# Kernel tuning notes

Measured on AMD Instinct MI355X. Metric: run time of the kernel, lower is better.

The kernel has to match this reference:

```python
import jax, jax.numpy as jnp
import numpy as np

N_EMBD = 1024
N_HEAD = 16
HEAD_SIZE = N_EMBD // N_HEAD
SEQ_LEN = 2048


def setup_inputs() -> dict:
    key = jax.random.key(0)
    k_x, k_wa, k_ba, k_wp, k_bp = jax.random.split(key, 5)
    s = 0.02
    return {
        "x": jax.random.normal(k_x, (4, SEQ_LEN, N_EMBD), dtype=jnp.float32),
        "w_attn": jax.random.normal(k_wa, (N_EMBD, 3 * N_EMBD), dtype=jnp.float32) * s,
        "b_attn": jax.random.normal(k_ba, (3 * N_EMBD,), dtype=jnp.float32) * s,
        "w_proj": jax.random.normal(k_wp, (N_EMBD, N_EMBD), dtype=jnp.float32) * s,
        "b_proj": jax.random.normal(k_bp, (N_EMBD,), dtype=jnp.float32) * s,
    }


def reference(x, w_attn, b_attn, w_proj, b_proj):
    B, T, C = x.shape
    H, D = N_HEAD, HEAD_SIZE
    qkv = x @ w_attn + b_attn                      # [B,T,3C]
    q, k, v = jnp.split(qkv, 3, axis=-1)
    q = q.reshape(B, T, H, D).transpose(0, 2, 1, 3)  # [B,H,T,D]
    k = k.reshape(B, T, H, D).transpose(0, 2, 1, 3)
    v = v.reshape(B, T, H, D).transpose(0, 2, 1, 3)
    att = jnp.einsum('bhqd,bhkd->bhqk', q, k) / jnp.sqrt(jnp.float32(D))
    causal = jnp.tril(jnp.ones((T, T), dtype=bool))
    att = jnp.where(causal[None, None], att, jnp.float32(-jnp.inf))
    att = jax.nn.softmax(att, axis=-1)
    out = jnp.einsum('bhqk,bhkd->bhqd', att, v)    # [B,H,T,D]
    out = out.transpose(0, 2, 1, 3).reshape(B, T, C)
    return out @ w_proj + b_proj
```

## Files before the change

### kernel.cpp

```cpp
#include <hip/hip_runtime.h>

typedef short short8 __attribute__((ext_vector_type(8)));
typedef short short4v __attribute__((ext_vector_type(4)));
typedef float f32x4 __attribute__((ext_vector_type(4)));
typedef unsigned uint2v __attribute__((ext_vector_type(2)));

__device__ __forceinline__ float bf2f(short b) {
  unsigned u = ((unsigned)(unsigned short)b) << 16;
  return __builtin_bit_cast(float, u);
}
__device__ __forceinline__ short f2bf(float f) {
  unsigned u = __builtin_bit_cast(unsigned, f);
  u += 0x7fffu + ((u >> 16) & 1u);
  return (short)(u >> 16);
}
__device__ __forceinline__ unsigned cvt_pk_bf16(float lo, float hi) {
  unsigned r;
  asm("v_cvt_pk_bf16_f32 %0, %1, %2" : "=v"(r) : "v"(lo), "v"(hi));
  return r;
}

__device__ __forceinline__ void gload_lds16(const void* g, void* l) {
  __builtin_amdgcn_global_load_lds(
      (const __attribute__((address_space(1))) unsigned int*)g,
      (__attribute__((address_space(3))) unsigned int*)l, 16, 0, 0);
}

__device__ __forceinline__ short8 lds_frag(const short* tile, int row, int kc, int l4) {
  int chunk = (kc * 4 + l4) ^ (row & 7);
  return *(const short8*)&tile[row * 64 + chunk * 8];
}

__global__ __launch_bounds__(256) void k_convert_bf16(const float* __restrict__ in,
                                                      short* __restrict__ out, int n8) {
  int i = blockIdx.x * 256 + threadIdx.x;
  if (i >= n8) return;
  const float4* p = (const float4*)in;
  float4 a = p[2 * i], b = p[2 * i + 1];
  short8 o;
  o[0] = f2bf(a.x); o[1] = f2bf(a.y); o[2] = f2bf(a.z); o[3] = f2bf(a.w);
  o[4] = f2bf(b.x); o[5] = f2bf(b.y); o[6] = f2bf(b.z); o[7] = f2bf(b.w);
  ((short8*)out)[i] = o;
}

__global__ __launch_bounds__(256) void k_transpose_w(const float* __restrict__ w,
                                                     short* __restrict__ wT, int K, int N) {
  __shared__ float t[32][33];
  int nt = N >> 5;
  int rt = blockIdx.x / nt, ct = blockIdx.x % nt;
  int tx = threadIdx.x & 31, ty = threadIdx.x >> 5;
#pragma unroll
  for (int i = 0; i < 4; ++i) {
    int r = ty * 4 + i;
    t[r][tx] = w[(size_t)(rt * 32 + r) * N + ct * 32 + tx];
  }
  __syncthreads();
#pragma unroll
  for (int i = 0; i < 4; ++i) {
    int r = ty * 4 + i;
    wT[(size_t)(ct * 32 + r) * K + rt * 32 + tx] = f2bf(t[tx][r]);
  }
}

template <bool BF16OUT>
__global__ __launch_bounds__(512, 1) void k_gemm8p(const short* __restrict__ A,
                                                   const short* __restrict__ Bt,
                                                   const float* __restrict__ bias,
                                                   void* __restrict__ Cout,
                                                   int M, int N, int K) {
  __shared__ __align__(16) short Ab[2][256 * 64];
  __shared__ __align__(16) short Bb[2][256 * 64];
  int nt = N >> 8;
  int nwg = gridDim.x;
  int bid = blockIdx.x;
  int swz = (bid & 7) * (nwg >> 3) + (bid >> 3);
  int mt = swz / nt, ct = swz % nt;
  int tid = threadIdx.x, w = tid >> 6, lane = tid & 63;
  int l15 = lane & 15, l4 = lane >> 4;
  int wm = w >> 2, wn = w & 3;
  const short* Abase = A + (size_t)mt * 256 * K;
  const short* Bbase = Bt + (size_t)ct * 256 * K;
  int NT = K >> 6;

  int srow = lane >> 3;
  int slc = (lane & 7) ^ srow;

  auto stage = [&](const short* gbase, short* dstTile, int kt, int half) {
#pragma unroll
    for (int i = 0; i < 2; ++i) {
      int rowg = half * 128 + i * 64 + w * 8;
      gload_lds16(gbase + (size_t)(rowg + srow) * K + kt * 64 + slc * 8,
                  dstTile + (size_t)rowg * 64);
    }
  };

  f32x4 acc[8][4];
#pragma unroll
  for (int m = 0; m < 8; ++m)
#pragma unroll
    for (int n = 0; n < 4; ++n) acc[m][n] = f32x4{0.f, 0.f, 0.f, 0.f};

  stage(Bbase, &Bb[0][0], 0, 0);
  stage(Bbase, &Bb[0][0], 0, 1);
  stage(Abase, &Ab[0][0], 0, 0);
  stage(Abase, &Ab[0][0], 0, 1);
  stage(Bbase, &Bb[1][0], 1, 0);
  stage(Bbase, &Bb[1][0], 1, 1);
  stage(Abase, &Ab[1][0], 1, 0);
  stage(Abase, &Ab[1][0], 1, 1);
  asm volatile("s_waitcnt vmcnt(8)" ::: "memory");
  __builtin_amdgcn_s_barrier();

  for (int t = 0; t < NT; ++t) {
    int b = t & 1;
    const short* At = &Ab[b][0];
    const short* Btl = &Bb[b][0];
    short* Aw = &Ab[b][0];
    short* Bw = &Bb[b][0];
    bool pre = (t + 2 < NT);

    short8 aflo[4][2], bflo[2][2], bfhi[2][2], afhi[4][2];
#pragma unroll
    for (int mq = 0; mq < 4; ++mq)
#pragma unroll
      for (int kc = 0; kc < 2; ++kc)
        aflo[mq][kc] = lds_frag(At, wm * 128 + mq * 16 + l15, kc, l4);
#pragma unroll
    for (int nq = 0; nq < 2; ++nq)
#pragma unroll
      for (int kc = 0; kc < 2; ++kc)
        bflo[nq][kc] = lds_frag(Btl, wn * 64 + nq * 16 + l15, kc, l4);
    __builtin_amdgcn_s_barrier();
    asm volatile("s_waitcnt lgkmcnt(0)" ::: "memory");
    __builtin_amdgcn_sched_barrier(0);
    __builtin_amdgcn_s_setprio(1);
#pragma unroll
    for (int mq = 0; mq < 4; ++mq)
#pragma unroll
      for (int nq = 0; nq < 2; ++nq)
#pragma unroll
        for (int kc = 0; kc < 2; ++kc)
          acc[mq][nq] = __builtin_amdgcn_mfma_f32_16x16x32_bf16(aflo[mq][kc], bflo[nq][kc], acc[mq][nq], 0, 0, 0);
    __builtin_amdgcn_s_setprio(0);
    __builtin_amdgcn_s_barrier();

#pragma unroll
    for (int nq = 0; nq < 2; ++nq)
#pragma unroll
      for (int kc = 0; kc < 2; ++kc)
        bfhi[nq][kc] = lds_frag(Btl, wn * 64 + 32 + nq * 16 + l15, kc, l4);
    __builtin_amdgcn_s_barrier();
    asm volatile("s_waitcnt lgkmcnt(0)" ::: "memory");
    __builtin_amdgcn_sched_barrier(0);
    __builtin_amdgcn_s_setprio(1);
#pragma unroll
    for (int mq = 0; mq < 4; ++mq)
#pragma unroll
      for (int nq = 0; nq < 2; ++nq)
#pragma unroll
        for (int kc = 0; kc < 2; ++kc)
          acc[mq][2 + nq] = __builtin_amdgcn_mfma_f32_16x16x32_bf16(aflo[mq][kc], bfhi[nq][kc], acc[mq][2 + nq], 0, 0, 0);
    __builtin_amdgcn_s_setprio(0);
    __builtin_amdgcn_s_barrier();

#pragma unroll
    for (int mq = 0; mq < 4; ++mq)
#pragma unroll
      for (int kc = 0; kc < 2; ++kc)
        afhi[mq][kc] = lds_frag(At, wm * 128 + 64 + mq * 16 + l15, kc, l4);
    if (pre) {
      stage(Bbase, Bw, t + 2, 0);
      stage(Bbase, Bw, t + 2, 1);
    }
    __builtin_amdgcn_s_barrier();
    asm volatile("s_waitcnt lgkmcnt(0)" ::: "memory");
    __builtin_amdgcn_sched_barrier(0);
    __builtin_amdgcn_s_setprio(1);
#pragma unroll
    for (int mq = 0; mq < 4; ++mq)
#pragma unroll
      for (int nq = 0; nq < 2; ++nq)
#pragma unroll
        for (int kc = 0; kc < 2; ++kc)
          acc[4 + mq][2 + nq] = __builtin_amdgcn_mfma_f32_16x16x32_bf16(afhi[mq][kc], bfhi[nq][kc], acc[4 + mq][2 + nq], 0, 0, 0);
    __builtin_amdgcn_s_setprio(0);
    __builtin_amdgcn_s_barrier();

    if (pre) {
      stage(Abase, Aw, t + 2, 0);
      stage(Abase, Aw, t + 2, 1);
    }
    __builtin_amdgcn_s_setprio(1);
#pragma unroll
    for (int mq = 0; mq < 4; ++mq)
#pragma unroll
      for (int nq = 0; nq < 2; ++nq)
#pragma unroll
        for (int kc = 0; kc < 2; ++kc)
          acc[4 + mq][nq] = __builtin_amdgcn_mfma_f32_16x16x32_bf16(afhi[mq][kc], bflo[nq][kc], acc[4 + mq][nq], 0, 0, 0);
    __builtin_amdgcn_s_setprio(0);
    if (pre) {
      asm volatile("s_waitcnt vmcnt(8)" ::: "memory");
    } else if (t + 1 < NT) {
      asm volatile("s_waitcnt vmcnt(0)" ::: "memory");
    }
    __builtin_amdgcn_s_barrier();
  }

#pragma unroll
  for (int m = 0; m < 8; ++m) {
#pragma unroll
    for (int n = 0; n < 4; ++n) {
      int row = mt * 256 + wm * 128 + m * 16 + l4 * 4;
      int col = ct * 256 + wn * 64 + n * 16 + l15;
      float bv = bias[col];
#pragma unroll
      for (int j = 0; j < 4; ++j) {
        float v = acc[m][n][j] + bv;
        if constexpr (BF16OUT)
          ((short*)Cout)[(size_t)(row + j) * N + col] = f2bf(v);
        else
          ((float*)Cout)[(size_t)(row + j) * N + col] = v;
      }
    }
  }
}

template <bool BF16OUT>
__global__ __launch_bounds__(256) void k_gemm_bt(const short* __restrict__ A,
                                                 const short* __restrict__ Bt,
                                                 const float* __restrict__ bias,
                                                 void* __restrict__ Cout,
                                                 int M, int N, int K) {
  __shared__ __align__(16) short As[128 * 32];
  __shared__ __align__(16) short Bs[128 * 32];
  int nt = N >> 7;
  int mt = blockIdx.x / nt, ct = blockIdx.x % nt;
  int tid = threadIdx.x, w = tid >> 6, lane = tid & 63;
  int l15 = lane & 15, l4 = lane >> 4;
  int wr = (w >> 1) * 64, wc = (w & 1) * 64;
  const short* Abase = A + (size_t)mt * 128 * K;
  const short* Bbase = Bt + (size_t)ct * 128 * K;
  f32x4 acc[4][4];
#pragma unroll
  for (int m = 0; m < 4; ++m)
#pragma unroll
    for (int n = 0; n < 4; ++n) acc[m][n] = f32x4{0.f, 0.f, 0.f, 0.f};

  for (int kt = 0; kt < K; kt += 32) {
    __syncthreads();
#pragma unroll
    for (int i = 0; i < 2; ++i) {
      int idx = (w * 2 + i) * 64 + lane;
      gload_lds16(Abase + (size_t)(idx >> 2) * K + kt + (idx & 3) * 8, &As[(w * 2 + i) * 512]);
      gload_lds16(Bbase + (size_t)(idx >> 2) * K + kt + (idx & 3) * 8, &Bs[(w * 2 + i) * 512]);
    }
    __syncthreads();
    short8 af[4], bfr[4];
#pragma unroll
    for (int m = 0; m < 4; ++m) af[m] = *(const short8*)&As[(wr + m * 16 + l15) * 32 + l4 * 8];
#pragma unroll
    for (int n = 0; n < 4; ++n) bfr[n] = *(const short8*)&Bs[(wc + n * 16 + l15) * 32 + l4 * 8];
#pragma unroll
    for (int m = 0; m < 4; ++m)
#pragma unroll
      for (int n = 0; n < 4; ++n)
        acc[m][n] = __builtin_amdgcn_mfma_f32_16x16x32_bf16(af[m], bfr[n], acc[m][n], 0, 0, 0);
  }

#pragma unroll
  for (int m = 0; m < 4; ++m) {
#pragma unroll
    for (int n = 0; n < 4; ++n) {
      int row = mt * 128 + wr + m * 16 + l4 * 4;
      int col = ct * 128 + wc + n * 16 + l15;
      float bv = bias[col];
#pragma unroll
      for (int j = 0; j < 4; ++j) {
        float v = acc[m][n][j] + bv;
        if constexpr (BF16OUT)
          ((short*)Cout)[(size_t)(row + j) * N + col] = f2bf(v);
        else
          ((float*)Cout)[(size_t)(row + j) * N + col] = v;
      }
    }
  }
}

__global__ __launch_bounds__(256) void k_transpose_v(const short* __restrict__ qkv,
                                                     short* __restrict__ vT) {
  __shared__ __align__(16) short t[64][72];
  int blk = blockIdx.x;
  int tt = blk & 31, bh = blk >> 5;
  int batch = bh >> 4, h = bh & 15;
  int tid = threadIdx.x;
  const short* base = qkv + (size_t)(batch * 2048 + tt * 64) * 3072 + 2048 + h * 64;
#pragma unroll
  for (int rep = 0; rep < 2; ++rep) {
    int idx = rep * 256 + tid;
    int r = idx >> 3, dc = idx & 7;
    *(short8*)&t[r][dc * 8] = *(const short8*)(base + (size_t)r * 3072 + dc * 8);
  }
  __syncthreads();
  short* obase = vT + (size_t)bh * 64 * 2048 + tt * 64;
#pragma unroll
  for (int rep = 0; rep < 2; ++rep) {
    int idx = rep * 256 + tid;
    int d = idx >> 3, tc = idx & 7;
    short8 o;
#pragma unroll
    for (int i = 0; i < 8; ++i) o[i] = t[tc * 8 + i][d];
    *(short8*)(obase + (size_t)d * 2048 + tc * 8) = o;
  }
}

__global__ __launch_bounds__(256, 2) void k_attn(const short* __restrict__ qkv,
                                                 const short* __restrict__ vT,
                                                 short* __restrict__ out) {
  constexpr int T = 2048, C3 = 3072;
  __shared__ __align__(16) short Kl[2][64 * 72];
  __shared__ __align__(16) short P_lds[4][32 * 72];
  int bp = blockIdx.x & 7, bh = blockIdx.x >> 3;
  int batch = bh >> 4, h = bh & 15;
  int tid = threadIdx.x, w = tid >> 6, lane = tid & 63;
  int l15 = lane & 15, l4 = lane >> 4;

  int qt[2];
  qt[0] = 63 - (bp * 4 + w);
  qt[1] = bp * 4 + w;
  int lim[2] = {qt[0] >> 1, qt[1] >> 1};
  int ktb = (63 - bp * 4) >> 1;

  const short* kbase = qkv + (size_t)(batch * T) * C3 + 1024 + h * 64;
  const short* vbase = vT + (size_t)bh * 64 * T;

  int sr0 = tid >> 3, sr1 = 32 + (tid >> 3), sdc = (tid & 7) * 8;

  const float SCL = 0.18033688f;
  short8 qf[2][2][2];
#pragma unroll
  for (int t = 0; t < 2; ++t)
#pragma unroll
    for (int qc = 0; qc < 2; ++qc) {
      const short* qrow = qkv + (size_t)(batch * T + qt[t] * 32 + qc * 16 + l15) * C3 + h * 64;
#pragma unroll
      for (int kc = 0; kc < 2; ++kc) {
        short8 v = *(const short8*)(qrow + kc * 32 + l4 * 8);
#pragma unroll
        for (int i = 0; i < 8; ++i) v[i] = f2bf(bf2f(v[i]) * SCL);
        qf[t][qc][kc] = v;
      }
    }

  f32x4 o_[2][2][4];
  float l_[2][2];
#pragma unroll
  for (int t = 0; t < 2; ++t)
#pragma unroll
    for (int qc = 0; qc < 2; ++qc) {
      l_[t][qc] = 0.f;
#pragma unroll
      for (int dt = 0; dt < 4; ++dt) o_[t][qc][dt] = f32x4{0.f, 0.f, 0.f, 0.f};
    }

  {
    short8 a = *(const short8*)(kbase + (size_t)sr0 * C3 + sdc);
    short8 b = *(const short8*)(kbase + (size_t)sr1 * C3 + sdc);
    *(short8*)&Kl[0][sr0 * 72 + sdc] = a;
    *(short8*)&Kl[0][sr1 * 72 + sdc] = b;
  }
  __syncthreads();

  int cur = 0;
  for (int kt = 0; kt <= ktb; ++kt) {
    bool more = (kt < ktb);
    bool act0 = (kt <= lim[0]), act1 = (kt <= lim[1]);

    short8 pre0, pre1;
    if (more) {
      pre0 = *(const short8*)(kbase + (size_t)((kt + 1) * 64 + sr0) * C3 + sdc);
      pre1 = *(const short8*)(kbase + (size_t)((kt + 1) * 64 + sr1) * C3 + sdc);
    }

    const short* Kb = &Kl[cur][0];
    short8 kf[4][2];
#pragma unroll
    for (int kvt = 0; kvt < 4; ++kvt)
#pragma unroll
      for (int kc = 0; kc < 2; ++kc)
        kf[kvt][kc] = *(const short8*)(Kb + (kvt * 16 + l15) * 72 + kc * 32 + l4 * 8);

    short8 vf[4][2];
#pragma unroll
    for (int dt = 0; dt < 4; ++dt)
#pragma unroll
      for (int kc = 0; kc < 2; ++kc)
        vf[dt][kc] = *(const short8*)(vbase + (size_t)(dt * 16 + l15) * T + kt * 64 + kc * 32 + l4 * 8);

#pragma unroll
    for (int t = 0; t < 2; ++t) {
      bool act = (t == 0) ? act0 : act1;
      if (!act) continue;
      short* pb = &P_lds[w][0];

#pragma unroll
      for (int qc = 0; qc < 2; ++qc) {
        f32x4 s[4];
#pragma unroll
        for (int kvt = 0; kvt < 4; ++kvt) s[kvt] = f32x4{0.f, 0.f, 0.f, 0.f};
        __builtin_amdgcn_s_setprio(1);
#pragma unroll
        for (int kvt = 0; kvt < 4; ++kvt)
#pragma unroll
          for (int kc = 0; kc < 2; ++kc)
            s[kvt] = __builtin_amdgcn_mfma_f32_16x16x32_bf16(kf[kvt][kc], qf[t][qc][kc], s[kvt], 0, 0, 0);
        __builtin_amdgcn_s_setprio(0);

        if (kt == lim[t]) {
          int qg = qt[t] * 32 + qc * 16 + l15;
#pragma unroll
          for (int kvt = 0; kvt < 4; ++kvt)
#pragma unroll
            for (int j = 0; j < 4; ++j) {
              int kg = kt * 64 + kvt * 16 + l4 * 4 + j;
              if (kg > qg) s[kvt][j] = -1e30f;
            }
        }

        float ls = 0.f;
#pragma unroll
        for (int kvt = 0; kvt < 4; ++kvt) {
          float p0 = exp2f(s[kvt][0]);
          float p1 = exp2f(s[kvt][1]);
          float p2 = exp2f(s[kvt][2]);
          float p3 = exp2f(s[kvt][3]);
          ls += (p0 + p1) + (p2 + p3);
          unsigned lo = cvt_pk_bf16(p0, p1);
          unsigned hi = cvt_pk_bf16(p2, p3);
          *(uint2v*)(pb + (qc * 16 + l15) * 72 + kvt * 16 + l4 * 4) = uint2v{lo, hi};
        }
        l_[t][qc] += ls;
      }

      asm volatile("s_waitcnt lgkmcnt(0)" ::: "memory");

      __builtin_amdgcn_s_setprio(1);
#pragma unroll
      for (int qc = 0; qc < 2; ++qc)
#pragma unroll
        for (int dt = 0; dt < 4; ++dt)
#pragma unroll
          for (int kc = 0; kc < 2; ++kc) {
            short8 pf = *(const short8*)(pb + (qc * 16 + l15) * 72 + kc * 32 + l4 * 8);
            o_[t][qc][dt] = __builtin_amdgcn_mfma_f32_16x16x32_bf16(vf[dt][kc], pf, o_[t][qc][dt], 0, 0, 0);
          }
      __builtin_amdgcn_s_setprio(0);
    }

    if (more) {
      *(short8*)&Kl[cur ^ 1][sr0 * 72 + sdc] = pre0;
      *(short8*)&Kl[cur ^ 1][sr1 * 72 + sdc] = pre1;
    }
    __syncthreads();
    cur ^= 1;
  }

#pragma unroll
  for (int t = 0; t < 2; ++t) {
#pragma unroll
    for (int qc = 0; qc < 2; ++qc) {
      float lt = l_[t][qc];
      lt += __shfl_xor(lt, 16);
      lt += __shfl_xor(lt, 32);
      float inv = 1.f / lt;
      size_t rowb = (size_t)(batch * T + qt[t] * 32 + qc * 16 + l15) * 1024 + h * 64;
#pragma unroll
      for (int dt = 0; dt < 4; ++dt) {
        short4v pk4;
#pragma unroll
        for (int j = 0; j < 4; ++j) pk4[j] = f2bf(o_[t][qc][dt][j] * inv);
        *(short4v*)(out + rowb + dt * 16 + l4 * 4) = pk4;
      }
    }
  }
}

extern "C" void kernel_launch(void* const* d_in, const int* in_sizes, int n_in,
                              void* d_out, int out_size, void* d_ws, size_t ws_size,
                              hipStream_t stream) {
  const float* x      = (const float*)d_in[0];
  const float* w_attn = (const float*)d_in[1];
  const float* b_attn = (const float*)d_in[2];
  const float* w_proj = (const float*)d_in[3];
  const float* b_proj = (const float*)d_in[4];
  float* out = (float*)d_out;

  char* ws = (char*)d_ws;
  short* xb   = (short*)(ws);
  short* waT  = (short*)(ws + 16777216);
  short* wpT  = (short*)(ws + 23068672);
  short* qkv  = (short*)(ws + 25165824);
  short* vT   = (short*)(ws + 75497472);
  short* attn = xb;

  k_convert_bf16<<<4096, 256, 0, stream>>>(x, xb, 1048576);
  k_transpose_w<<<32 * 96, 256, 0, stream>>>(w_attn, waT, 1024, 3072);
  k_transpose_w<<<32 * 32, 256, 0, stream>>>(w_proj, wpT, 1024, 1024);
  k_gemm8p<true><<<384, 512, 0, stream>>>(xb, waT, b_attn, qkv, 8192, 3072, 1024);
  k_transpose_v<<<2048, 256, 0, stream>>>(qkv, vT);
  k_attn<<<512, 256, 0, stream>>>(qkv, vT, attn);
  k_gemm_bt<false><<<64 * 8, 256, 0, stream>>>(attn, wpT, b_proj, out, 8192, 1024, 1024);
}
```

Before: 199.1 us.

## Halve attention query tile per wave and double block count for occupancy

Each wave in the attention kernel now processes 16-row query tiles instead of 32. The grid doubles to 1024 blocks, and launch bounds now allow 4 blocks per CU. Fewer accumulator registers and more resident waves are meant to improve latency hiding and load balance across CUs. The cost is more K/V tile loads from memory per query row, since each loaded tile feeds half as many queries.

```diff
diff --git a/kernel.cpp b/kernel.cpp
--- a/kernel.cpp
+++ b/kernel.cpp
@@ -314,22 +314,23 @@
   }
 }
 
-__global__ __launch_bounds__(256, 2) void k_attn(const short* __restrict__ qkv,
+__global__ __launch_bounds__(256, 4) void k_attn(const short* __restrict__ qkv,
                                                  const short* __restrict__ vT,
                                                  short* __restrict__ out) {
   constexpr int T = 2048, C3 = 3072;
   __shared__ __align__(16) short Kl[2][64 * 72];
-  __shared__ __align__(16) short P_lds[4][32 * 72];
-  int bp = blockIdx.x & 7, bh = blockIdx.x >> 3;
+  __shared__ __align__(16) short P_lds[4][16 * 72];
+  int bp = blockIdx.x & 15, bh = blockIdx.x >> 4;
   int batch = bh >> 4, h = bh & 15;
   int tid = threadIdx.x, w = tid >> 6, lane = tid & 63;
   int l15 = lane & 15, l4 = lane >> 4;
 
+  int x = bp * 4 + w;
   int qt[2];
-  qt[0] = 63 - (bp * 4 + w);
-  qt[1] = bp * 4 + w;
-  int lim[2] = {qt[0] >> 1, qt[1] >> 1};
-  int ktb = (63 - bp * 4) >> 1;
+  qt[0] = 127 - x;
+  qt[1] = x;
+  int lim[2] = {(qt[0] * 16 + 15) >> 6, (qt[1] * 16 + 15) >> 6};
+  int ktb = 31 - bp;
 
   const short* kbase = qkv + (size_t)(batch * T) * C3 + 1024 + h * 64;
   const short* vbase = vT + (size_t)bh * 64 * T;
@@ -337,31 +338,25 @@
   int sr0 = tid >> 3, sr1 = 32 + (tid >> 3), sdc = (tid & 7) * 8;
 
   const float SCL = 0.18033688f;
-  short8 qf[2][2][2];
+  short8 qf[2][2];
+#pragma unroll
+  for (int t = 0; t < 2; ++t) {
+    const short* qrow = qkv + (size_t)(batch * T + qt[t] * 16 + l15) * C3 + h * 64;
+#pragma unroll
+    for (int kc = 0; kc < 2; ++kc) {
+      short8 v = *(const short8*)(qrow + kc * 32 + l4 * 8);
+#pragma unroll
+      for (int i = 0; i < 8; ++i) v[i] = f2bf(bf2f(v[i]) * SCL);
+      qf[t][kc] = v;
+    }
+  }
+
+  f32x4 o_[2][4];
+  float l_[2] = {0.f, 0.f};
 #pragma unroll
   for (int t = 0; t < 2; ++t)
 #pragma unroll
-    for (int qc = 0; qc < 2; ++qc) {
-      const short* qrow = qkv + (size_t)(batch * T + qt[t] * 32 + qc * 16 + l15) * C3 + h * 64;
-#pragma unroll
-      for (int kc = 0; kc < 2; ++kc) {
-        short8 v = *(const short8*)(qrow + kc * 32 + l4 * 8);
-#pragma unroll
-        for (int i = 0; i < 8; ++i) v[i] = f2bf(bf2f(v[i]) * SCL);
-        qf[t][qc][kc] = v;
-      }
-    }
-
-  f32x4 o_[2][2][4];
-  float l_[2][2];
-#pragma unroll
-  for (int t = 0; t < 2; ++t)
-#pragma unroll
-    for (int qc = 0; qc < 2; ++qc) {
-      l_[t][qc] = 0.f;
-#pragma unroll
-      for (int dt = 0; dt < 4; ++dt) o_[t][qc][dt] = f32x4{0.f, 0.f, 0.f, 0.f};
-    }
+    for (int dt = 0; dt < 4; ++dt) o_[t][dt] = f32x4{0.f, 0.f, 0.f, 0.f};
 
   {
     short8 a = *(const short8*)(kbase + (size_t)sr0 * C3 + sdc);
@@ -397,63 +392,58 @@
       for (int kc = 0; kc < 2; ++kc)
         vf[dt][kc] = *(const short8*)(vbase + (size_t)(dt * 16 + l15) * T + kt * 64 + kc * 32 + l4 * 8);
 
+    short* pb = &P_lds[w][0];
 #pragma unroll
     for (int t = 0; t < 2; ++t) {
       bool act = (t == 0) ? act0 : act1;
       if (!act) continue;
-      short* pb = &P_lds[w][0];
-
-#pragma unroll
-      for (int qc = 0; qc < 2; ++qc) {
-        f32x4 s[4];
-#pragma unroll
-        for (int kvt = 0; kvt < 4; ++kvt) s[kvt] = f32x4{0.f, 0.f, 0.f, 0.f};
-        __builtin_amdgcn_s_setprio(1);
+
+      f32x4 s[4];
+#pragma unroll
+      for (int kvt = 0; kvt < 4; ++kvt) s[kvt] = f32x4{0.f, 0.f, 0.f, 0.f};
+      __builtin_amdgcn_s_setprio(1);
+#pragma unroll
+      for (int kvt = 0; kvt < 4; ++kvt)
+#pragma unroll
+        for (int kc = 0; kc < 2; ++kc)
+          s[kvt] = __builtin_amdgcn_mfma_f32_16x16x32_bf16(kf[kvt][kc], qf[t][kc], s[kvt], 0, 0, 0);
+      __builtin_amdgcn_s_setprio(0);
+
+      if (kt == lim[t]) {
+        int qg = qt[t] * 16 + l15;
 #pragma unroll
         for (int kvt = 0; kvt < 4; ++kvt)
 #pragma unroll
-          for (int kc = 0; kc < 2; ++kc)
-            s[kvt] = __builtin_amdgcn_mfma_f32_16x16x32_bf16(kf[kvt][kc], qf[t][qc][kc], s[kvt], 0, 0, 0);
-        __builtin_amdgcn_s_setprio(0);
-
-        if (kt == lim[t]) {
-          int qg = qt[t] * 32 + qc * 16 + l15;
-#pragma unroll
-          for (int kvt = 0; kvt < 4; ++kvt)
-#pragma unroll
-            for (int j = 0; j < 4; ++j) {
-              int kg = kt * 64 + kvt * 16 + l4 * 4 + j;
-              if (kg > qg) s[kvt][j] = -1e30f;
-            }
+          for (int j = 0; j < 4; ++j) {
+            int kg = kt * 64 + kvt * 16 + l4 * 4 + j;
+            if (kg > qg) s[kvt][j] = -1e30f;
+          }
+      }
+
+      float ls = 0.f;
+#pragma unroll
+      for (int kvt = 0; kvt < 4; ++kvt) {
+        float p0 = exp2f(s[kvt][0]);
+        float p1 = exp2f(s[kvt][1]);
+        float p2 = exp2f(s[kvt][2]);
+        float p3 = exp2f(s[kvt][3]);
+        ls += (p0 + p1) + (p2 + p3);
+        unsigned lo = cvt_pk_bf16(p0, p1);
+        unsigned hi = cvt_pk_bf16(p2, p3);
+        *(uint2v*)(pb + l15 * 72 + kvt * 16 + l4 * 4) = uint2v{lo, hi};
+      }
+      l_[t] += ls;
+
+      asm volatile("s_waitcnt lgkmcnt(0)" ::: "memory");
+
+      __builtin_amdgcn_s_setprio(1);
+#pragma unroll
+      for (int dt = 0; dt < 4; ++dt)
+#pragma unroll
+        for (int kc = 0; kc < 2; ++kc) {
+          short8 pf = *(const short8*)(pb + l15 * 72 + kc * 32 + l4 * 8);
+          o_[t][dt] = __builtin_amdgcn_mfma_f32_16x16x32_bf16(vf[dt][kc], pf, o_[t][dt], 0, 0, 0);
         }
-
-        float ls = 0.f;
-#pragma unroll
-        for (int kvt = 0; kvt < 4; ++kvt) {
-          float p0 = exp2f(s[kvt][0]);
-          float p1 = exp2f(s[kvt][1]);
-          float p2 = exp2f(s[kvt][2]);
-          float p3 = exp2f(s[kvt][3]);
-          ls += (p0 + p1) + (p2 + p3);
-          unsigned lo = cvt_pk_bf16(p0, p1);
-          unsigned hi = cvt_pk_bf16(p2, p3);
-          *(uint2v*)(pb + (qc * 16 + l15) * 72 + kvt * 16 + l4 * 4) = uint2v{lo, hi};
-        }
-        l_[t][qc] += ls;
-      }
-
-      asm volatile("s_waitcnt lgkmcnt(0)" ::: "memory");
-
-      __builtin_amdgcn_s_setprio(1);
-#pragma unroll
-      for (int qc = 0; qc < 2; ++qc)
-#pragma unroll
-        for (int dt = 0; dt < 4; ++dt)
-#pragma unroll
-          for (int kc = 0; kc < 2; ++kc) {
-            short8 pf = *(const short8*)(pb + (qc * 16 + l15) * 72 + kc * 32 + l4 * 8);
-            o_[t][qc][dt] = __builtin_amdgcn_mfma_f32_16x16x32_bf16(vf[dt][kc], pf, o_[t][qc][dt], 0, 0, 0);
-          }
       __builtin_amdgcn_s_setprio(0);
     }
 
@@ -467,20 +457,17 @@
 
 #pragma unroll
   for (int t = 0; t < 2; ++t) {
-#pragma unroll
-    for (int qc = 0; qc < 2; ++qc) {
-      float lt = l_[t][qc];
-      lt += __shfl_xor(lt, 16);
-      lt += __shfl_xor(lt, 32);
-      float inv = 1.f / lt;
-      size_t rowb = (size_t)(batch * T + qt[t] * 32 + qc * 16 + l15) * 1024 + h * 64;
-#pragma unroll
-      for (int dt = 0; dt < 4; ++dt) {
-        short4v pk4;
-#pragma unroll
-        for (int j = 0; j < 4; ++j) pk4[j] = f2bf(o_[t][qc][dt][j] * inv);
-        *(short4v*)(out + rowb + dt * 16 + l4 * 4) = pk4;
-      }
+    float lt = l_[t];
+    lt += __shfl_xor(lt, 16);
+    lt += __shfl_xor(lt, 32);
+    float inv = 1.f / lt;
+    size_t rowb = (size_t)(batch * T + qt[t] * 16 + l15) * 1024 + h * 64;
+#pragma unroll
+    for (int dt = 0; dt < 4; ++dt) {
+      short4v pk4;
+#pragma unroll
+      for (int j = 0; j < 4; ++j) pk4[j] = f2bf(o_[t][dt][j] * inv);
+      *(short4v*)(out + rowb + dt * 16 + l4 * 4) = pk4;
     }
   }
 }
@@ -508,6 +495,6 @@
   k_transpose_w<<<32 * 32, 256, 0, stream>>>(w_proj, wpT, 1024, 1024);
   k_gemm8p<true><<<384, 512, 0, stream>>>(xb, waT, b_attn, qkv, 8192, 3072, 1024);
   k_transpose_v<<<2048, 256, 0, stream>>>(qkv, vT);
-  k_attn<<<512, 256, 0, stream>>>(qkv, vT, attn);
+  k_attn<<<1024, 256, 0, stream>>>(qkv, vT, attn);
   k_gemm_bt<false><<<64 * 8, 256, 0, stream>>>(attn, wpT, b_proj, out, 8192, 1024, 1024);
 }
```

After: 336.8 us. 1.69x slower.
